# Performance work log

Measured on AMD Instinct MI355X. Metric: run time of the kernel, lower is better.

## Reference

```python
import jax, jax.numpy as jnp
import numpy as np

B, Q, K, DQ, DK, H, DV = 4, 512, 512, 512, 512, 256, 512


def setup_inputs() -> dict:
    key = jax.random.key(0)
    ks = jax.random.split(key, 9)
    return {
        "query": jax.random.normal(ks[0], (B, Q, DQ), dtype=jnp.float32),
        "key": jax.random.normal(ks[1], (B, K, DK), dtype=jnp.float32),
        "value": jax.random.normal(ks[2], (B, K, DV), dtype=jnp.float32),
        "Wq": jax.random.normal(ks[3], (DQ, H), dtype=jnp.float32) / np.sqrt(DQ),
        "bq": jax.random.normal(ks[4], (H,), dtype=jnp.float32) * 0.01,
        "Wk": jax.random.normal(ks[5], (DK, H), dtype=jnp.float32) / np.sqrt(DK),
        "bk": jax.random.normal(ks[6], (H,), dtype=jnp.float32) * 0.01,
        "wv": jax.random.normal(ks[7], (H,), dtype=jnp.float32) / np.sqrt(H),
        "bv": jax.random.normal(ks[8], (), dtype=jnp.float32) * 0.01,
    }


def reference(query, key, value, Wq, bq, Wk, bk, wv, bv):
    # Projections: [B,Q,H] and [B,K,H]
    q = jnp.einsum("bqd,dh->bqh", query, Wq) + bq
    k = jnp.einsum("bkd,dh->bkh", key, Wk) + bk
    # Broadcast add + tanh: [B,Q,K,H] (the large intermediate)
    feat = jnp.tanh(q[:, :, None, :] + k[:, None, :, :])
    # Linear-to-scalar score: [B,Q,K]
    score = jnp.einsum("bqkh,h->bqk", feat, wv) + bv
    attention_weight = jax.nn.softmax(score, axis=-1)
    # Dropout is identity at eval; weighted sum over keys: [B,Q,DV]
    context = jnp.einsum("bqk,bkd->bqd", attention_weight, value)
    return (context, attention_weight)
```

## Files before the change

kernel.cpp:

```cpp
#include <hip/hip_runtime.h>
#include <hip/hip_bf16.h>

#define B_ 4
#define Q_ 512
#define K_ 512
#define DQ_ 512
#define H_ 256
#define DV_ 512

#define SC2 2.8853900817779268f

typedef unsigned short u16;
typedef short bf16x8 __attribute__((ext_vector_type(8)));
typedef float f32x4 __attribute__((ext_vector_type(4)));
typedef float f32x2 __attribute__((ext_vector_type(2)));
typedef unsigned short u16x4 __attribute__((ext_vector_type(4)));

__device__ __forceinline__ unsigned bsplit(float a) {
    unsigned u  = __float_as_uint(a);
    unsigned hi = (u + 0x7FFFu + ((u >> 16) & 1u)) >> 16;
    float hf = __uint_as_float(hi << 16);
    float l  = a - hf;
    unsigned ul = __float_as_uint(l);
    unsigned lo = (ul + 0x7FFFu + ((ul >> 16) & 1u)) >> 16;
    return (hi << 16) | lo;
}

__device__ __forceinline__ void gld16(const void* g, void* l) {
    __builtin_amdgcn_global_load_lds(
        (const __attribute__((address_space(1))) unsigned int*)g,
        (__attribute__((address_space(3))) unsigned int*)l, 16, 0, 0);
}

__global__ __launch_bounds__(256) void cvt_rows(
    const float* __restrict__ query, const float* __restrict__ key,
    u16* __restrict__ qA_hi, u16* __restrict__ qA_lo)
{
    const int z = blockIdx.y;
    const float* src = z ? key : query;
    u16* dh = qA_hi + (long long)z * 1048576;
    u16* dl = qA_lo + (long long)z * 1048576;
    long long i4 = (long long)blockIdx.x * 256 + threadIdx.x;
    float4 v = ((const float4*)src)[i4];
    unsigned a = bsplit(v.x), b = bsplit(v.y), c = bsplit(v.z), d = bsplit(v.w);
    u16x4 h4 = {(u16)(a >> 16), (u16)(b >> 16), (u16)(c >> 16), (u16)(d >> 16)};
    u16x4 l4 = {(u16)(a & 0xFFFF), (u16)(b & 0xFFFF), (u16)(c & 0xFFFF), (u16)(d & 0xFFFF)};
    *(u16x4*)(dh + i4 * 4) = h4;
    *(u16x4*)(dl + i4 * 4) = l4;
}

__global__ __launch_bounds__(256) void cvt_T(
    const float* __restrict__ Wq, const float* __restrict__ Wk,
    const float* __restrict__ value,
    u16* __restrict__ WT_hi, u16* __restrict__ WT_lo,
    u16* __restrict__ vT_hi, u16* __restrict__ vT_lo)
{
    __shared__ float t[32][33];
    const int z = blockIdx.z;
    const int x = threadIdx.x, y = threadIdx.y;
    const float* src; u16 *dh, *dl; int C;
    if (z < 2) {
        if (blockIdx.y >= 8) return;
        src = z ? Wk : Wq; C = 256;
        dh = WT_hi + (long long)z * 131072;
        dl = WT_lo + (long long)z * 131072;
    } else {
        src = value + (long long)(z - 2) * 262144; C = 512;
        dh = vT_hi + (long long)(z - 2) * 262144;
        dl = vT_lo + (long long)(z - 2) * 262144;
    }
    const int r0 = blockIdx.x * 32, c0 = blockIdx.y * 32;
    #pragma unroll
    for (int i = 0; i < 32; i += 8)
        t[y + i][x] = src[(long long)(r0 + y + i) * C + c0 + x];
    __syncthreads();
    #pragma unroll
    for (int i = 0; i < 32; i += 8) {
        unsigned p = bsplit(t[x][y + i]);
        long long o = (long long)(c0 + y + i) * 512 + r0 + x;
        dh[o] = (u16)(p >> 16);
        dl[o] = (u16)(p & 0xFFFF);
    }
}

__global__ __launch_bounds__(256) void mfma_gemm(
    const u16* __restrict__ Ah0, const u16* __restrict__ Al0,
    const u16* __restrict__ Bh0, const u16* __restrict__ Bl0,
    const float* __restrict__ biasq, const float* __restrict__ biask,
    float* __restrict__ outp, int mode, int Kd,
    long long sA, long long sB, long long sO)
{
    const int z = blockIdx.z;
    const u16* Ah = Ah0 + z * sA;
    const u16* Al = Al0 + z * sA;
    const u16* Bh = Bh0 + z * sB;
    const u16* Bl = Bl0 + z * sB;

    const int m0 = blockIdx.x * 64;
    const int n0 = blockIdx.y * 64;

    __shared__ u16 AhS[64 * 64], AlS[64 * 64], BhS[64 * 64], BlS[64 * 64];

    const int tid = threadIdx.x;
    const int lane = tid & 63, w = tid >> 6;
    const int wr = w >> 1, wc = w & 1;
    const int lrow = lane & 15, lgrp = lane >> 4;

    f32x4 acc[2][2] = {};

    for (int k0 = 0; k0 < Kd; k0 += 64) {
        #pragma unroll
        for (int it = 0; it < 2; ++it) {
            int idx = tid + it * 256;
            int row = idx >> 3, u = idx & 7;
            long long go = (long long)(m0 + row) * Kd + k0 + ((u ^ (row & 7)) << 3);
            long long gb = (long long)(n0 + row) * Kd + k0 + ((u ^ (row & 7)) << 3);
            gld16(Ah + go, AhS + idx * 8);
            gld16(Al + go, AlS + idx * 8);
            gld16(Bh + gb, BhS + idx * 8);
            gld16(Bl + gb, BlS + idx * 8);
        }
        __syncthreads();

        #pragma unroll
        for (int kk = 0; kk < 2; ++kk) {
            bf16x8 ah[2], al[2], bh[2], bl[2];
            #pragma unroll
            for (int f = 0; f < 2; ++f) {
                int ar = wr * 32 + f * 16 + lrow;
                int au = (kk * 4 + lgrp) ^ (ar & 7);
                ah[f] = *(const bf16x8*)(AhS + ar * 64 + au * 8);
                al[f] = *(const bf16x8*)(AlS + ar * 64 + au * 8);
                int br = wc * 32 + f * 16 + lrow;
                int bu = (kk * 4 + lgrp) ^ (br & 7);
                bh[f] = *(const bf16x8*)(BhS + br * 64 + bu * 8);
                bl[f] = *(const bf16x8*)(BlS + br * 64 + bu * 8);
            }
            #pragma unroll
            for (int fm = 0; fm < 2; ++fm)
                #pragma unroll
                for (int fn = 0; fn < 2; ++fn) {
                    acc[fm][fn] = __builtin_amdgcn_mfma_f32_16x16x32_bf16(ah[fm], bh[fn], acc[fm][fn], 0, 0, 0);
                    acc[fm][fn] = __builtin_amdgcn_mfma_f32_16x16x32_bf16(ah[fm], bl[fn], acc[fm][fn], 0, 0, 0);
                    acc[fm][fn] = __builtin_amdgcn_mfma_f32_16x16x32_bf16(al[fm], bh[fn], acc[fm][fn], 0, 0, 0);
                }
        }
        __syncthreads();
    }

    if (mode == 0) {
        const float* bs = z ? biask : biasq;
        #pragma unroll
        for (int fm = 0; fm < 2; ++fm)
            #pragma unroll
            for (int fn = 0; fn < 2; ++fn)
                #pragma unroll
                for (int r = 0; r < 4; ++r) {
                    int m = m0 + wr * 32 + fm * 16 + lgrp * 4 + r;
                    int n = n0 + wc * 32 + fn * 16 + lrow;
                    float v = __builtin_amdgcn_exp2f((acc[fm][fn][r] + bs[n]) * SC2);
                    if (z == 0) {
                        outp[(((long long)(m >> 2) * H_ + n) << 2) + (m & 3)] = v;
                    } else {
                        int bb = m >> 9, k = m & 511;
                        outp[sO + (((long long)(bb * 64 + (n >> 2)) * 512 + k) << 2) + (n & 3)] = v;
                    }
                }
    } else {
        float* C = outp + (long long)z * sO;
        #pragma unroll
        for (int fm = 0; fm < 2; ++fm)
            #pragma unroll
            for (int fn = 0; fn < 2; ++fn)
                #pragma unroll
                for (int r = 0; r < 4; ++r) {
                    int m = m0 + wr * 32 + fm * 16 + lgrp * 4 + r;
                    int n = n0 + wc * 32 + fn * 16 + lrow;
                    C[(long long)m * DV_ + n] = acc[fm][fn][r];
                }
    }
}

#define QT 4

__global__ __launch_bounds__(1024) void score_softmax(
    const float* __restrict__ qp4E,
    const float* __restrict__ kT4E,
    const float* __restrict__ wv,
    float* __restrict__ attn_out,
    u16* __restrict__ aB_hi, u16* __restrict__ aB_lo)
{
    const int b   = blockIdx.y;
    const int q0  = blockIdx.x * QT;
    const int tid = threadIdx.x;
    const int k16 = tid & 255;
    const int qtr = tid >> 8;
    const int lane = tid & 63;

    __shared__ float lq[H_][QT];
    __shared__ float lwv[H_];
    __shared__ float pacc[3][2][256][4];
    __shared__ float red[4][QT];

    if (tid < H_) {
        const float4* qsrc = (const float4*)qp4E + ((long long)(b * (Q_ / 4) + blockIdx.x)) * H_;
        *(float4*)&lq[tid][0] = qsrc[tid];
    } else if (tid < 2 * H_) {
        lwv[tid - H_] = wv[tid - H_];
    }
    __syncthreads();

    f32x2 a01[2] = {{0.f,0.f},{0.f,0.f}}, a23[2] = {{0.f,0.f},{0.f,0.f}};
    const float4* kvec = (const float4*)kT4E + (long long)b * (H_ / 4) * K_ + k16;
    const int g0 = qtr * 16;

    #pragma unroll 2
    for (int gi = 0; gi < 16; ++gi) {
        const int g = g0 + gi;
        float4 kA = kvec[(long long)g * K_];
        float4 kB = kvec[(long long)g * K_ + 256];
        float4 w4 = *(const float4*)&lwv[g * 4];
        float kAa[4] = {kA.x, kA.y, kA.z, kA.w};
        float kBa[4] = {kB.x, kB.y, kB.z, kB.w};
        float wa[4]  = {w4.x, w4.y, w4.z, w4.w};
        #pragma unroll
        for (int u = 0; u < 4; ++u) {
            float4 q4 = *(const float4*)&lq[(g << 2) + u][0];
            f32x2 Eq01 = {q4.x, q4.y}, Eq23 = {q4.z, q4.w};
            const f32x2 one = {1.f, 1.f};
            f32x2 wu = {wa[u], wa[u]};
            f32x2 eA = {kAa[u], kAa[u]}, eB = {kBa[u], kBa[u]};
            f32x2 dA01 = __builtin_elementwise_fma(Eq01, eA, one);
            f32x2 dA23 = __builtin_elementwise_fma(Eq23, eA, one);
            f32x2 dB01 = __builtin_elementwise_fma(Eq01, eB, one);
            f32x2 dB23 = __builtin_elementwise_fma(Eq23, eB, one);
            f32x2 rA01 = {__builtin_amdgcn_rcpf(dA01.x), __builtin_amdgcn_rcpf(dA01.y)};
            f32x2 rA23 = {__builtin_amdgcn_rcpf(dA23.x), __builtin_amdgcn_rcpf(dA23.y)};
            f32x2 rB01 = {__builtin_amdgcn_rcpf(dB01.x), __builtin_amdgcn_rcpf(dB01.y)};
            f32x2 rB23 = {__builtin_amdgcn_rcpf(dB23.x), __builtin_amdgcn_rcpf(dB23.y)};
            a01[0] = __builtin_elementwise_fma(rA01, wu, a01[0]);
            a23[0] = __builtin_elementwise_fma(rA23, wu, a23[0]);
            a01[1] = __builtin_elementwise_fma(rB01, wu, a01[1]);
            a23[1] = __builtin_elementwise_fma(rB23, wu, a23[1]);
        }
    }

    if (qtr) {
        #pragma unroll
        for (int kk = 0; kk < 2; ++kk) {
            float4 v = make_float4(a01[kk].x, a01[kk].y, a23[kk].x, a23[kk].y);
            *(float4*)&pacc[qtr - 1][kk][k16][0] = v;
        }
    }
    __syncthreads();

    float s[2][QT], e[2][QT], mx[QT];
    if (!qtr) {
        #pragma unroll
        for (int kk = 0; kk < 2; ++kk) {
            float4 t0 = *(const float4*)&pacc[0][kk][k16][0];
            float4 t1 = *(const float4*)&pacc[1][kk][k16][0];
            float4 t2 = *(const float4*)&pacc[2][kk][k16][0];
            s[kk][0] = -2.f * (a01[kk].x + t0.x + t1.x + t2.x);
            s[kk][1] = -2.f * (a01[kk].y + t0.y + t1.y + t2.y);
            s[kk][2] = -2.f * (a23[kk].x + t0.z + t1.z + t2.z);
            s[kk][3] = -2.f * (a23[kk].y + t0.w + t1.w + t2.w);
        }
        #pragma unroll
        for (int qq = 0; qq < QT; ++qq) {
            float v = fmaxf(s[0][qq], s[1][qq]);
            #pragma unroll
            for (int off = 32; off; off >>= 1) v = fmaxf(v, __shfl_xor(v, off));
            if (lane == 0) red[tid >> 6][qq] = v;
        }
    }
    __syncthreads();
    if (!qtr) {
        #pragma unroll
        for (int qq = 0; qq < QT; ++qq)
            mx[qq] = fmaxf(fmaxf(red[0][qq], red[1][qq]), fmaxf(red[2][qq], red[3][qq]));
    }
    __syncthreads();
    if (!qtr) {
        #pragma unroll
        for (int qq = 0; qq < QT; ++qq) {
            e[0][qq] = __expf(s[0][qq] - mx[qq]);
            e[1][qq] = __expf(s[1][qq] - mx[qq]);
            float v = e[0][qq] + e[1][qq];
            #pragma unroll
            for (int off = 32; off; off >>= 1) v += __shfl_xor(v, off);
            if (lane == 0) red[tid >> 6][qq] = v;
        }
    }
    __syncthreads();
    if (!qtr) {
        #pragma unroll
        for (int qq = 0; qq < QT; ++qq) {
            float v = red[0][qq] + red[1][qq] + red[2][qq] + red[3][qq];
            float rv = __builtin_amdgcn_rcpf(v);
            #pragma unroll
            for (int kk = 0; kk < 2; ++kk) {
                float a = e[kk][qq] * rv;
                long long o = (long long)(b * Q_ + q0 + qq) * K_ + k16 + kk * 256;
                attn_out[o] = a;
                unsigned p = bsplit(a);
                aB_hi[o] = (u16)(p >> 16);
                aB_lo[o] = (u16)(p & 0xFFFF);
            }
        }
    }
}

extern "C" void kernel_launch(void* const* d_in, const int* in_sizes, int n_in,
                              void* d_out, int out_size, void* d_ws, size_t ws_size,
                              hipStream_t stream) {
    const float* query = (const float*)d_in[0];
    const float* key   = (const float*)d_in[1];
    const float* value = (const float*)d_in[2];
    const float* Wq    = (const float*)d_in[3];
    const float* bq    = (const float*)d_in[4];
    const float* Wk    = (const float*)d_in[5];
    const float* bk    = (const float*)d_in[6];
    const float* wv    = (const float*)d_in[7];

    float* out = (float*)d_out;
    float* ctx_out  = out;
    float* attn_out = out + (size_t)B_ * Q_ * DV_;

    float* ws   = (float*)d_ws;
    float* qp4  = ws;
    float* kT4  = qp4 + 524288;
    u16* qA_hi  = (u16*)(kT4 + 524288);
    u16* kA_hi  = qA_hi + 1048576;
    u16* qA_lo  = kA_hi + 1048576;
    u16* kA_lo  = qA_lo + 1048576;
    u16* WqT_hi = kA_lo + 1048576;
    u16* WkT_hi = WqT_hi + 131072;
    u16* WqT_lo = WkT_hi + 131072;
    u16* WkT_lo = WqT_lo + 131072;
    u16* vT_hi  = WkT_lo + 131072;
    u16* vT_lo  = vT_hi + 1048576;
    u16* aB_hi  = vT_lo + 1048576;
    u16* aB_lo  = aB_hi + 1048576;
    (void)qA_lo; (void)WqT_lo; (void)n_in; (void)ws_size; (void)in_sizes; (void)out_size;

    hipLaunchKernelGGL(cvt_rows, dim3(1024, 2), dim3(256), 0, stream,
                       query, key, qA_hi, qA_lo);
    hipLaunchKernelGGL(cvt_T, dim3(16, 16, 6), dim3(32, 8), 0, stream,
                       Wq, Wk, value, WqT_hi, WqT_lo, vT_hi, vT_lo);

    hipLaunchKernelGGL(mfma_gemm, dim3(32, 4, 2), dim3(256), 0, stream,
                       qA_hi, qA_lo, WqT_hi, WqT_lo, bq, bk, qp4, 0, 512,
                       (long long)1048576, (long long)131072, (long long)524288);

    hipLaunchKernelGGL(score_softmax, dim3(Q_ / QT, B_), dim3(1024), 0, stream,
                       qp4, kT4, wv, attn_out, aB_hi, aB_lo);

    hipLaunchKernelGGL(mfma_gemm, dim3(8, 8, 4), dim3(256), 0, stream,
                       aB_hi, aB_lo, vT_hi, vT_lo, (const float*)nullptr, (const float*)nullptr,
                       ctx_out, 2, 512,
                       (long long)262144, (long long)262144, (long long)262144);
}
```

Before: 73.20 us.

## Merge pairs of rational terms to halve reciprocals in score loop

```diff
diff --git a/kernel.cpp b/kernel.cpp
--- a/kernel.cpp
+++ b/kernel.cpp
@@ -30,6 +30,21 @@
     __builtin_amdgcn_global_load_lds(
         (const __attribute__((address_space(1))) unsigned int*)g,
         (__attribute__((address_space(3))) unsigned int*)l, 16, 0, 0);
+}
+
+__device__ __forceinline__ void pair_acc(
+    f32x2 Eq0, f32x2 Eq1, float ek0, float ek1,
+    float w0, float w1, float w01, f32x2& acc)
+{
+    f32x2 e0 = Eq0 * (f32x2){ek0, ek0};
+    f32x2 e1 = Eq1 * (f32x2){ek1, ek1};
+    f32x2 s  = e0 + e1;
+    f32x2 den = __builtin_elementwise_fma(e0, e1, s);
+    den = den + (f32x2){1.f, 1.f};
+    f32x2 num = __builtin_elementwise_fma(e1, (f32x2){w0, w0}, (f32x2){w01, w01});
+    num = __builtin_elementwise_fma(e0, (f32x2){w1, w1}, num);
+    f32x2 r = {__builtin_amdgcn_rcpf(den.x), __builtin_amdgcn_rcpf(den.y)};
+    acc = __builtin_elementwise_fma(num, r, acc);
 }
 
 __global__ __launch_bounds__(256) void cvt_rows(
@@ -198,15 +213,17 @@
     const int lane = tid & 63;
 
     __shared__ float lq[H_][QT];
-    __shared__ float lwv[H_];
+    __shared__ float lwp[H_ / 2][4];
     __shared__ float pacc[3][2][256][4];
     __shared__ float red[4][QT];
 
     if (tid < H_) {
         const float4* qsrc = (const float4*)qp4E + ((long long)(b * (Q_ / 4) + blockIdx.x)) * H_;
         *(float4*)&lq[tid][0] = qsrc[tid];
-    } else if (tid < 2 * H_) {
-        lwv[tid - H_] = wv[tid - H_];
+    } else if (tid < H_ + H_ / 2) {
+        int p = tid - H_;
+        float w0 = wv[2 * p], w1 = wv[2 * p + 1];
+        lwp[p][0] = w0; lwp[p][1] = w1; lwp[p][2] = w0 + w1; lwp[p][3] = 0.f;
     }
     __syncthreads();
 
@@ -214,35 +231,36 @@
     const float4* kvec = (const float4*)kT4E + (long long)b * (H_ / 4) * K_ + k16;
     const int g0 = qtr * 16;
 
+    float4 kA = kvec[(long long)g0 * K_];
+    float4 kB = kvec[(long long)g0 * K_ + 256];
     #pragma unroll 2
     for (int gi = 0; gi < 16; ++gi) {
         const int g = g0 + gi;
-        float4 kA = kvec[(long long)g * K_];
-        float4 kB = kvec[(long long)g * K_ + 256];
-        float4 w4 = *(const float4*)&lwv[g * 4];
-        float kAa[4] = {kA.x, kA.y, kA.z, kA.w};
-        float kBa[4] = {kB.x, kB.y, kB.z, kB.w};
-        float wa[4]  = {w4.x, w4.y, w4.z, w4.w};
-        #pragma unroll
-        for (int u = 0; u < 4; ++u) {
-            float4 q4 = *(const float4*)&lq[(g << 2) + u][0];
-            f32x2 Eq01 = {q4.x, q4.y}, Eq23 = {q4.z, q4.w};
-            const f32x2 one = {1.f, 1.f};
-            f32x2 wu = {wa[u], wa[u]};
-            f32x2 eA = {kAa[u], kAa[u]}, eB = {kBa[u], kBa[u]};
-            f32x2 dA01 = __builtin_elementwise_fma(Eq01, eA, one);
-            f32x2 dA23 = __builtin_elementwise_fma(Eq23, eA, one);
-            f32x2 dB01 = __builtin_elementwise_fma(Eq01, eB, one);
-            f32x2 dB23 = __builtin_elementwise_fma(Eq23, eB, one);
-            f32x2 rA01 = {__builtin_amdgcn_rcpf(dA01.x), __builtin_amdgcn_rcpf(dA01.y)};
-            f32x2 rA23 = {__builtin_amdgcn_rcpf(dA23.x), __builtin_amdgcn_rcpf(dA23.y)};
-            f32x2 rB01 = {__builtin_amdgcn_rcpf(dB01.x), __builtin_amdgcn_rcpf(dB01.y)};
-            f32x2 rB23 = {__builtin_amdgcn_rcpf(dB23.x), __builtin_amdgcn_rcpf(dB23.y)};
-            a01[0] = __builtin_elementwise_fma(rA01, wu, a01[0]);
-            a23[0] = __builtin_elementwise_fma(rA23, wu, a23[0]);
-            a01[1] = __builtin_elementwise_fma(rB01, wu, a01[1]);
-            a23[1] = __builtin_elementwise_fma(rB23, wu, a23[1]);
-        }
+        float4 kAc = kA, kBc = kB;
+        if (gi < 15) {
+            kA = kvec[(long long)(g + 1) * K_];
+            kB = kvec[(long long)(g + 1) * K_ + 256];
+        }
+        float4 q4_0 = *(const float4*)&lq[(g << 2) + 0][0];
+        float4 q4_1 = *(const float4*)&lq[(g << 2) + 1][0];
+        float4 q4_2 = *(const float4*)&lq[(g << 2) + 2][0];
+        float4 q4_3 = *(const float4*)&lq[(g << 2) + 3][0];
+        float4 wp0 = *(const float4*)&lwp[(g << 1) + 0][0];
+        float4 wp1 = *(const float4*)&lwp[(g << 1) + 1][0];
+
+        f32x2 q0_01 = {q4_0.x, q4_0.y}, q0_23 = {q4_0.z, q4_0.w};
+        f32x2 q1_01 = {q4_1.x, q4_1.y}, q1_23 = {q4_1.z, q4_1.w};
+        f32x2 q2_01 = {q4_2.x, q4_2.y}, q2_23 = {q4_2.z, q4_2.w};
+        f32x2 q3_01 = {q4_3.x, q4_3.y}, q3_23 = {q4_3.z, q4_3.w};
+
+        pair_acc(q0_01, q1_01, kAc.x, kAc.y, wp0.x, wp0.y, wp0.z, a01[0]);
+        pair_acc(q0_23, q1_23, kAc.x, kAc.y, wp0.x, wp0.y, wp0.z, a23[0]);
+        pair_acc(q2_01, q3_01, kAc.z, kAc.w, wp1.x, wp1.y, wp1.z, a01[0]);
+        pair_acc(q2_23, q3_23, kAc.z, kAc.w, wp1.x, wp1.y, wp1.z, a23[0]);
+        pair_acc(q0_01, q1_01, kBc.x, kBc.y, wp0.x, wp0.y, wp0.z, a01[1]);
+        pair_acc(q0_23, q1_23, kBc.x, kBc.y, wp0.x, wp0.y, wp0.z, a23[1]);
+        pair_acc(q2_01, q3_01, kBc.z, kBc.w, wp1.x, wp1.y, wp1.z, a01[1]);
+        pair_acc(q2_23, q3_23, kBc.z, kBc.w, wp1.x, wp1.y, wp1.z, a23[1]);
     }
 
     if (qtr) {
```

After: 72.59 us. Within noise of the previous version (-0.8%).
